# Kernel tuning notes

Measured on AMD Instinct MI355X. Metric: run time of the kernel, lower is better.

## Reference

```python
import jax, jax.numpy as jnp
import numpy as np

GRID = 9          # 9x9 taxi grid -> 81 zones
N_ZONES = GRID * GRID
OBS_DIM = 48      # obs[:, :48] used by every zone's dense layer
MAX_ADJ = 5       # self + up/down/left/right
BATCH = 32768
NEG_INF = -1e9


def _grid_adjacency():
    """Padded adjacency (self + valid 4-neighbors) for a 9x9 grid."""
    idx = np.zeros((N_ZONES, MAX_ADJ), dtype=np.int32)
    mask = np.zeros((N_ZONES, MAX_ADJ), dtype=np.float32)
    for i in range(N_ZONES):
        r, c = divmod(i, GRID)
        nbrs = [i]
        if r > 0: nbrs.append(i - GRID)
        if r < GRID - 1: nbrs.append(i + GRID)
        if c > 0: nbrs.append(i - 1)
        if c < GRID - 1: nbrs.append(i + 1)
        for j, n in enumerate(nbrs):
            idx[i, j] = n
            mask[i, j] = 1.0
    return idx, mask


def setup_inputs() -> dict:
    key = jax.random.key(0)
    k_obs, k_w = jax.random.split(key)
    obs = jax.random.normal(k_obs, (BATCH, OBS_DIM), dtype=jnp.float32)
    # per-zone dense weights [48 -> adjacent_num], padded to MAX_ADJ
    W = jax.random.normal(k_w, (N_ZONES, OBS_DIM, MAX_ADJ), dtype=jnp.float32) * 0.1
    b = jnp.zeros((N_ZONES, MAX_ADJ), dtype=jnp.float32)
    idx_np, mask_np = _grid_adjacency()
    return {"obs": obs, "W": W, "b": b,
            "idx": jnp.asarray(idx_np), "mask": jnp.asarray(mask_np)}


def reference(obs, W, b, idx, mask):
    x = obs[:, :OBS_DIM]                              # [B, 48]
    # batched tiny GEMMs: one [48 -> K] dense per zone
    logits = jnp.einsum('bd,ndk->bnk', x, W) + b      # [B, N, K]
    logits = jnp.where(mask > 0, logits, NEG_INF)     # padded slots -> 0 after softmax
    probs = jax.nn.softmax(logits, axis=-1) * mask    # [B, N, K]
    B = obs.shape[0]
    n, k = idx.shape
    rows = jnp.broadcast_to(jnp.arange(n)[:, None], (n, k))  # zone index per slot
    out = jnp.zeros((B, n, N_ZONES), dtype=obs.dtype)
    # scatter each zone's softmax probs into its adjacency positions of an 81-vector
    out = out.at[:, rows, idx].add(probs)
    return out                                        # [B, 81, 81]
```

## Files before the change

kernel.cpp:

```cpp
#include <hip/hip_runtime.h>

#define NZ 81
#define OBS_DIM 48
#define MAX_ADJ 5
#define NTASK (NZ * MAX_ADJ)
#define TPAD 408
#define NEG_INF -1000000000.0f
#define BLOCK 512
#define ROWS 16
#define CHUNK 4
#define NCHUNK (ROWS / CHUNK)
#define ROW_DW (NZ * NZ)
#define NPOS 13

__global__ __launch_bounds__(BLOCK) void taxi_actor_kernel(
    const float* __restrict__ obs,
    const float* __restrict__ W,
    const float* __restrict__ bias,
    const int*   __restrict__ idx,
    const float* __restrict__ mask,
    float* __restrict__ out)
{
    __shared__ float s_obs[ROWS * OBS_DIM];
    __shared__ float s_lp[CHUNK][TPAD];
    __shared__ int   s_idx[NTASK];

    const int tid = threadIdx.x;
    const size_t b0 = (size_t)blockIdx.x * ROWS;

    if (tid < ROWS * OBS_DIM / 4) {
        const float4* src = reinterpret_cast<const float4*>(obs + b0 * OBS_DIM);
        reinterpret_cast<float4*>(s_obs)[tid] = src[tid];
    }
    if (tid < NTASK)
        s_idx[tid] = (mask[tid] > 0.0f) ? idx[tid] : -1;
    __syncthreads();

    int tmap[NPOS];
    #pragma unroll
    for (int i = 0; i < NPOS; ++i) {
        tmap[i] = -1;
        const int p = tid + i * BLOCK;
        if (p < ROW_DW) {
            const int n = p / NZ;
            const int z = p - n * NZ;
            #pragma unroll
            for (int k = 0; k < MAX_ADJ; ++k)
                if (s_idx[n * MAX_ADJ + k] == z) tmap[i] = n * MAX_ADJ + k;
        }
    }

    const float* __restrict__ Wp = W;
    float bv = 0.0f;
    bool valid = false;
    const int n0 = tid / MAX_ADJ;
    const int k0 = tid - n0 * MAX_ADJ;
    if (tid < NTASK) {
        Wp = W + n0 * (OBS_DIM * MAX_ADJ) + k0;
        bv = bias[tid];
        valid = (s_idx[tid] >= 0);
    }

    for (int c = 0; c < NCHUNK; ++c) {
        const int rb = c * CHUNK;

        float a0 = 0.f, a1 = 0.f, a2 = 0.f, a3 = 0.f;
        if (tid < NTASK) {
            #pragma unroll
            for (int d4 = 0; d4 < OBS_DIM; d4 += 4) {
                const float w0 = Wp[(d4 + 0) * MAX_ADJ];
                const float w1 = Wp[(d4 + 1) * MAX_ADJ];
                const float w2 = Wp[(d4 + 2) * MAX_ADJ];
                const float w3 = Wp[(d4 + 3) * MAX_ADJ];
                const float4 o0 = *reinterpret_cast<const float4*>(&s_obs[(rb + 0) * OBS_DIM + d4]);
                const float4 o1 = *reinterpret_cast<const float4*>(&s_obs[(rb + 1) * OBS_DIM + d4]);
                const float4 o2 = *reinterpret_cast<const float4*>(&s_obs[(rb + 2) * OBS_DIM + d4]);
                const float4 o3 = *reinterpret_cast<const float4*>(&s_obs[(rb + 3) * OBS_DIM + d4]);
                a0 = fmaf(o0.x, w0, a0); a0 = fmaf(o0.y, w1, a0); a0 = fmaf(o0.z, w2, a0); a0 = fmaf(o0.w, w3, a0);
                a1 = fmaf(o1.x, w0, a1); a1 = fmaf(o1.y, w1, a1); a1 = fmaf(o1.z, w2, a1); a1 = fmaf(o1.w, w3, a1);
                a2 = fmaf(o2.x, w0, a2); a2 = fmaf(o2.y, w1, a2); a2 = fmaf(o2.z, w2, a2); a2 = fmaf(o2.w, w3, a2);
                a3 = fmaf(o3.x, w0, a3); a3 = fmaf(o3.y, w1, a3); a3 = fmaf(o3.z, w2, a3); a3 = fmaf(o3.w, w3, a3);
            }
        }
        __syncthreads();
        if (tid < NTASK) {
            s_lp[0][tid] = valid ? (a0 + bv) : NEG_INF;
            s_lp[1][tid] = valid ? (a1 + bv) : NEG_INF;
            s_lp[2][tid] = valid ? (a2 + bv) : NEG_INF;
            s_lp[3][tid] = valid ? (a3 + bv) : NEG_INF;
        }
        __syncthreads();

        if (tid < CHUNK * NZ) {
            const int r = tid / NZ;
            const int n = tid - r * NZ;
            float l[MAX_ADJ];
            float m = NEG_INF;
            #pragma unroll
            for (int k = 0; k < MAX_ADJ; ++k) {
                l[k] = s_lp[r][n * MAX_ADJ + k];
                m = fmaxf(m, l[k]);
            }
            float ssum = 0.0f;
            #pragma unroll
            for (int k = 0; k < MAX_ADJ; ++k) {
                l[k] = __expf(l[k] - m);
                ssum += l[k];
            }
            const float inv = 1.0f / ssum;
            #pragma unroll
            for (int k = 0; k < MAX_ADJ; ++k)
                s_lp[r][n * MAX_ADJ + k] = l[k] * inv;
        }
        __syncthreads();

        #pragma unroll
        for (int r = 0; r < CHUNK; ++r) {
            float* __restrict__ ob = out + (b0 + rb + r) * (size_t)ROW_DW;
            #pragma unroll
            for (int i = 0; i < NPOS; ++i) {
                const int p = tid + i * BLOCK;
                if (p < ROW_DW)
                    ob[p] = (tmap[i] >= 0) ? s_lp[r][tmap[i]] : 0.0f;
            }
        }
    }
}

extern "C" void kernel_launch(void* const* d_in, const int* in_sizes, int n_in,
                              void* d_out, int out_size, void* d_ws, size_t ws_size,
                              hipStream_t stream) {
    const float* obs  = (const float*)d_in[0];
    const float* W    = (const float*)d_in[1];
    const float* bias = (const float*)d_in[2];
    const int*   idx  = (const int*)d_in[3];
    const float* mask = (const float*)d_in[4];
    float* out = (float*)d_out;

    const int B = in_sizes[0] / OBS_DIM;
    taxi_actor_kernel<<<B / ROWS, BLOCK, 0, stream>>>(obs, W, bias, idx, mask, out);
}
```

Before: 221.2 us.

## Double-buffer logits and store scatter map in shared memory

Adds a second shared-memory buffer for chunk logits, so the next chunk's GEMV and softmax are issued after the current chunk's output stores, with fewer barriers per chunk. The per-thread 13-entry tmap register array becomes a shared short array that is read once per output position. The store loop is reordered to loop over rows for each position. The aim is to overlap the long global write stream with compute and to free registers for occupancy, at the cost of extra LDS traffic and more shared memory.

Result: slower. 319.3 us (+44.3%).

```diff
diff --git a/kernel.cpp b/kernel.cpp
--- a/kernel.cpp
+++ b/kernel.cpp
@@ -22,8 +22,9 @@
     float* __restrict__ out)
 {
     __shared__ float s_obs[ROWS * OBS_DIM];
-    __shared__ float s_lp[CHUNK][TPAD];
+    __shared__ float s_lp[2][CHUNK][TPAD];
     __shared__ int   s_idx[NTASK];
+    __shared__ short s_map[ROW_DW + 7];
 
     const int tid = threadIdx.x;
     const size_t b0 = (size_t)blockIdx.x * ROWS;
@@ -36,36 +37,32 @@
         s_idx[tid] = (mask[tid] > 0.0f) ? idx[tid] : -1;
     __syncthreads();
 
-    int tmap[NPOS];
-    #pragma unroll
-    for (int i = 0; i < NPOS; ++i) {
-        tmap[i] = -1;
-        const int p = tid + i * BLOCK;
-        if (p < ROW_DW) {
-            const int n = p / NZ;
-            const int z = p - n * NZ;
-            #pragma unroll
-            for (int k = 0; k < MAX_ADJ; ++k)
-                if (s_idx[n * MAX_ADJ + k] == z) tmap[i] = n * MAX_ADJ + k;
-        }
+    for (int p = tid; p < ROW_DW; p += BLOCK) {
+        const int n = p / NZ;
+        const int z = p - n * NZ;
+        short t = -1;
+        #pragma unroll
+        for (int k = 0; k < MAX_ADJ; ++k)
+            if (s_idx[n * MAX_ADJ + k] == z) t = (short)(n * MAX_ADJ + k);
+        s_map[p] = t;
     }
 
     const float* __restrict__ Wp = W;
     float bv = 0.0f;
     bool valid = false;
-    const int n0 = tid / MAX_ADJ;
-    const int k0 = tid - n0 * MAX_ADJ;
     if (tid < NTASK) {
-        Wp = W + n0 * (OBS_DIM * MAX_ADJ) + k0;
+        const int n = tid / MAX_ADJ;
+        const int k = tid - n * MAX_ADJ;
+        Wp = W + n * (OBS_DIM * MAX_ADJ) + k;
         bv = bias[tid];
-        valid = (s_idx[tid] >= 0);
+        valid = (mask[tid] > 0.0f);
     }
 
-    for (int c = 0; c < NCHUNK; ++c) {
-        const int rb = c * CHUNK;
-
-        float a0 = 0.f, a1 = 0.f, a2 = 0.f, a3 = 0.f;
+    auto compute_chunk = [&](int c) {
         if (tid < NTASK) {
+            const int rb = c * CHUNK;
+            const int buf = c & 1;
+            float a0 = 0.f, a1 = 0.f, a2 = 0.f, a3 = 0.f;
             #pragma unroll
             for (int d4 = 0; d4 < OBS_DIM; d4 += 4) {
                 const float w0 = Wp[(d4 + 0) * MAX_ADJ];
@@ -81,24 +78,23 @@
                 a2 = fmaf(o2.x, w0, a2); a2 = fmaf(o2.y, w1, a2); a2 = fmaf(o2.z, w2, a2); a2 = fmaf(o2.w, w3, a2);
                 a3 = fmaf(o3.x, w0, a3); a3 = fmaf(o3.y, w1, a3); a3 = fmaf(o3.z, w2, a3); a3 = fmaf(o3.w, w3, a3);
             }
+            s_lp[buf][0][tid] = valid ? (a0 + bv) : NEG_INF;
+            s_lp[buf][1][tid] = valid ? (a1 + bv) : NEG_INF;
+            s_lp[buf][2][tid] = valid ? (a2 + bv) : NEG_INF;
+            s_lp[buf][3][tid] = valid ? (a3 + bv) : NEG_INF;
         }
-        __syncthreads();
-        if (tid < NTASK) {
-            s_lp[0][tid] = valid ? (a0 + bv) : NEG_INF;
-            s_lp[1][tid] = valid ? (a1 + bv) : NEG_INF;
-            s_lp[2][tid] = valid ? (a2 + bv) : NEG_INF;
-            s_lp[3][tid] = valid ? (a3 + bv) : NEG_INF;
-        }
-        __syncthreads();
+    };
 
+    auto softmax_chunk = [&](int c) {
         if (tid < CHUNK * NZ) {
+            const int buf = c & 1;
             const int r = tid / NZ;
             const int n = tid - r * NZ;
             float l[MAX_ADJ];
             float m = NEG_INF;
             #pragma unroll
             for (int k = 0; k < MAX_ADJ; ++k) {
-                l[k] = s_lp[r][n * MAX_ADJ + k];
+                l[k] = s_lp[buf][r][n * MAX_ADJ + k];
                 m = fmaxf(m, l[k]);
             }
             float ssum = 0.0f;
@@ -110,19 +106,40 @@
             const float inv = 1.0f / ssum;
             #pragma unroll
             for (int k = 0; k < MAX_ADJ; ++k)
-                s_lp[r][n * MAX_ADJ + k] = l[k] * inv;
+                s_lp[buf][r][n * MAX_ADJ + k] = l[k] * inv;
         }
-        __syncthreads();
+    };
 
-        #pragma unroll
-        for (int r = 0; r < CHUNK; ++r) {
-            float* __restrict__ ob = out + (b0 + rb + r) * (size_t)ROW_DW;
+    compute_chunk(0);
+    __syncthreads();
+    softmax_chunk(0);
+    __syncthreads();
+
+    for (int c = 0; c < NCHUNK; ++c) {
+        const int buf = c & 1;
+
+        {
+            const size_t rbase = b0 + (size_t)c * CHUNK;
             #pragma unroll
             for (int i = 0; i < NPOS; ++i) {
                 const int p = tid + i * BLOCK;
-                if (p < ROW_DW)
-                    ob[p] = (tmap[i] >= 0) ? s_lp[r][tmap[i]] : 0.0f;
+                if (p < ROW_DW) {
+                    const short t = s_map[p];
+                    #pragma unroll
+                    for (int r = 0; r < CHUNK; ++r) {
+                        float v = 0.0f;
+                        if (t >= 0) v = s_lp[buf][r][t];
+                        out[(rbase + r) * (size_t)ROW_DW + p] = v;
+                    }
+                }
             }
+        }
+
+        if (c + 1 < NCHUNK) {
+            compute_chunk(c + 1);
+            __syncthreads();
+            softmax_chunk(c + 1);
+            __syncthreads();
         }
     }
 }
```
